# Kernel tuning notes

Hardware: AMD Instinct MI355X
Metric: run time of the kernel (lower is better)

Reference implementation:

```python
import jax, jax.numpy as jnp
import numpy as np


def _sq_cdist(x, y):
    # x: [B,N,D], y: [B,M,D] -> squared L2 distances [B,N,M]
    x_norm = jnp.sum(x * x, axis=-1, keepdims=True)          # [B,N,1]
    y_norm = jnp.sum(y * y, axis=-1, keepdims=True)          # [B,M,1]
    xy = jnp.einsum('bnd,bmd->bnm', x, y)                    # [B,N,M]
    return x_norm - 2.0 * xy + jnp.swapaxes(y_norm, -2, -1)  # [B,N,M]


def setup_inputs() -> dict:
    key = jax.random.key(0)
    kx, ky = jax.random.split(key)
    B, N, M, D = 8, 8192, 8192, 3
    x = jax.random.normal(kx, (B, N, D), dtype=jnp.float32)
    y = jax.random.normal(ky, (B, M, D), dtype=jnp.float32)
    return {"x": x, "y": y}


def reference(x, y):
    d = _sq_cdist(x, y)  # [B,N,M] squared distances (no sqrt, matching original)
    # original d was [B,M,N]; min(dim=2)->per-y-point min over N, min(dim=1)->per-x-point min over M
    per_y = jnp.min(d, axis=1)  # [B,M]
    per_x = jnp.min(d, axis=2)  # [B,N]
    return jnp.mean(per_y) + jnp.mean(per_x)
```

## Files before the change

kernel.cpp:

```cpp
#include <hip/hip_runtime.h>
#include <math.h>


#define B_      8
#define N_      8192
#define Q_      4
#define S_      16
#define CHUNK_  (N_ / S_)


__global__ __launch_bounds__(256)
void minpass_kernel(const float* __restrict__ x, const float* __restrict__ y,
                    float* __restrict__ partX, float* __restrict__ partY) {
    __shared__ float4 sq[CHUNK_];

    const int b    = blockIdx.y;
    const int z    = blockIdx.z;
    const int pass = z >> 4;
    const int s    = z & (S_ - 1);

    const float* qpts = pass ? y : x;
    const float* tpts = pass ? x : y;
    float*       part = pass ? partY : partX;

    {
        const float* tb = tpts + ((long)b * N_ + s * CHUNK_) * 3;
        const float* p  = tb + 6 * threadIdx.x;
        float a0 = p[0], a1 = p[1], a2 = p[2];
        float a3 = p[3], a4 = p[4], a5 = p[5];
        sq[2 * threadIdx.x + 0] = make_float4(-2.0f * a0, -2.0f * a1, -2.0f * a2,
                                              fmaf(a0, a0, fmaf(a1, a1, a2 * a2)));
        sq[2 * threadIdx.x + 1] = make_float4(-2.0f * a3, -2.0f * a4, -2.0f * a5,
                                              fmaf(a3, a3, fmaf(a4, a4, a5 * a5)));
    }
    __syncthreads();

    const int iq0 = (blockIdx.x * blockDim.x + threadIdx.x) * Q_;
    const float4* qp4 = (const float4*)(qpts + ((long)b * N_ + iq0) * 3);
    const float4 f0 = qp4[0];
    const float4 f1 = qp4[1];
    const float4 f2 = qp4[2];
    const float qx[Q_] = {f0.x, f0.w, f1.z, f2.y};
    const float qy[Q_] = {f0.y, f1.x, f1.w, f2.z};
    const float qz[Q_] = {f0.z, f1.y, f2.x, f2.w};

    float m[Q_];
#pragma unroll
    for (int i = 0; i < Q_; ++i) m[i] = __builtin_inff();

    for (int j = 0; j < CHUNK_; j += 4) {
        const float4 ta = sq[j + 0];
        const float4 tb = sq[j + 1];
        const float4 tc = sq[j + 2];
        const float4 td = sq[j + 3];
#pragma unroll
        for (int i = 0; i < Q_; ++i) {
            float sa = fmaf(qx[i], ta.x, fmaf(qy[i], ta.y, fmaf(qz[i], ta.z, ta.w)));
            float sb = fmaf(qx[i], tb.x, fmaf(qy[i], tb.y, fmaf(qz[i], tb.z, tb.w)));
            float sc = fmaf(qx[i], tc.x, fmaf(qy[i], tc.y, fmaf(qz[i], tc.z, tc.w)));
            float sd = fmaf(qx[i], td.x, fmaf(qy[i], td.y, fmaf(qz[i], td.z, td.w)));
            float t  = fminf(fminf(sa, sb), sc);
            m[i]     = fminf(fminf(t, sd), m[i]);
        }
    }

    float4 d;
    {
        float xn0 = fmaf(qx[0], qx[0], fmaf(qy[0], qy[0], qz[0] * qz[0]));
        float xn1 = fmaf(qx[1], qx[1], fmaf(qy[1], qy[1], qz[1] * qz[1]));
        float xn2 = fmaf(qx[2], qx[2], fmaf(qy[2], qy[2], qz[2] * qz[2]));
        float xn3 = fmaf(qx[3], qx[3], fmaf(qy[3], qy[3], qz[3] * qz[3]));
        d.x = fmaxf(m[0] + xn0, 0.0f);
        d.y = fmaxf(m[1] + xn1, 0.0f);
        d.z = fmaxf(m[2] + xn2, 0.0f);
        d.w = fmaxf(m[3] + xn3, 0.0f);
    }
    *(float4*)(part + (long)s * (B_ * N_) + (long)b * N_ + iq0) = d;
}

__global__ __launch_bounds__(256)
void merge_kernel(const float* __restrict__ partX, const float* __restrict__ partY,
                  float* __restrict__ bsum, int BN) {
    const int g = blockIdx.x * blockDim.x + threadIdx.x;
    const float* base = (g < BN) ? (partX + g) : (partY + (g - BN));

    float m = __builtin_inff();
#pragma unroll
    for (int s = 0; s < S_; ++s)
        m = fminf(m, base[(long)s * BN]);

    for (int off = 32; off > 0; off >>= 1)
        m += __shfl_down(m, off, 64);
    __shared__ float wsum[4];
    const int lane = threadIdx.x & 63;
    const int w    = threadIdx.x >> 6;
    if (lane == 0) wsum[w] = m;
    __syncthreads();
    if (threadIdx.x == 0)
        bsum[blockIdx.x] = (wsum[0] + wsum[1]) + (wsum[2] + wsum[3]);
}

__global__ __launch_bounds__(64)
void final_kernel(const float* __restrict__ bsum, float* __restrict__ out,
                  int nb, float scale) {
    float s = 0.0f;
    for (int k = threadIdx.x; k < nb; k += 64)
        s += bsum[k];
    for (int off = 32; off > 0; off >>= 1)
        s += __shfl_down(s, off, 64);
    if (threadIdx.x == 0) out[0] = s * scale;
}

extern "C" void kernel_launch(void* const* d_in, const int* in_sizes, int n_in,
                              void* d_out, int out_size, void* d_ws, size_t ws_size,
                              hipStream_t stream) {
    const float* x = (const float*)d_in[0];
    const float* y = (const float*)d_in[1];
    float* out = (float*)d_out;

    const int BN = B_ * N_;

    float* partX = (float*)d_ws;
    float* partY = partX + (size_t)S_ * BN;
    float* bsum  = partY + (size_t)S_ * BN;

    minpass_kernel<<<dim3(N_ / (256 * Q_), B_, 2 * S_), 256, 0, stream>>>(x, y, partX, partY);

    const int nb = 2 * BN / 256;
    merge_kernel<<<nb, 256, 0, stream>>>(partX, partY, bsum, BN);
    final_kernel<<<1, 64, 0, stream>>>(bsum, out, nb, 1.0f / 65536.0f);
}
```

Measured before the change: 139.9 us.

## Compute pairwise distance terms with split-bf16 MFMA instead of scalar FMAs

Moves the inner distance computation onto matrix cores. Each coordinate is split into bf16 hi/lo parts so the dot product and norm term are computed near fp32 precision with two 16x16x32 bf16 MFMAs per 16x16 tile. A prep kernel packs the target points into MFMA fragment layout in global memory, and the split count drops from 16 to 2, shrinking the merge pass. This risks small precision loss and wasted MFMA lanes, since most of the K dimension is zero padding, and it adds an extra kernel launch.

Measured after the change: 155.7 us. +11.3%, slower.

```diff
diff --git a/kernel.cpp b/kernel.cpp
--- a/kernel.cpp
+++ b/kernel.cpp
@@ -1,100 +1,154 @@
 #include <hip/hip_runtime.h>
 #include <math.h>
+#include <stdint.h>
 
 
-#define B_      8
-#define N_      8192
-#define Q_      4
-#define S_      16
-#define CHUNK_  (N_ / S_)
+#define B_  8
+#define N_  8192
 
+typedef short  s16x8 __attribute__((ext_vector_type(8)));
+typedef float  f32x4 __attribute__((ext_vector_type(4)));
+typedef int    i32x4 __attribute__((ext_vector_type(4)));
+
+__device__ __forceinline__ unsigned bf16rn(float f) {
+    unsigned u = __float_as_uint(f);
+    return (u + 0x7FFFu + ((u >> 16) & 1u)) >> 16;
+}
+__device__ __forceinline__ float bf16tof(unsigned h) {
+    return __uint_as_float(h << 16);
+}
+__device__ __forceinline__ int pk2(unsigned lo, unsigned hi) {
+    return (int)(lo | (hi << 16));
+}
+union frag_u { i32x4 i; s16x8 h; };
+__device__ __forceinline__ s16x8 mkfrag(int w0, int w1, int w2, int w3) {
+    frag_u u; u.i = (i32x4){w0, w1, w2, w3}; return u.h;
+}
+
+__global__ void prep_kernel(const float* __restrict__ x, const float* __restrict__ y,
+                            char* __restrict__ AX, char* __restrict__ AY) {
+    int i = blockIdx.x * blockDim.x + threadIdx.x;
+    if (i >= 2 * B_ * N_) return;
+    const float* src = (i < B_ * N_) ? x : y;
+    char* A = (i < B_ * N_) ? AX : AY;
+    int idx = i & (B_ * N_ - 1);
+    const float* p = src + (long)idx * 3;
+    float t0 = p[0], t1 = p[1], t2 = p[2];
+    float a0 = -2.f * t0, a1 = -2.f * t1, a2 = -2.f * t2;
+    unsigned h0 = bf16rn(a0), h1 = bf16rn(a1), h2 = bf16rn(a2);
+    unsigned l0 = bf16rn(a0 - bf16tof(h0));
+    unsigned l1 = bf16rn(a1 - bf16tof(h1));
+    unsigned l2 = bf16rn(a2 - bf16tof(h2));
+    float tn = fmaf(t0, t0, fmaf(t1, t1, t2 * t2));
+    unsigned nh = bf16rn(tn);
+    unsigned nl = bf16rn(tn - bf16tof(nh));
+    int tile = idx >> 4, r = idx & 15;
+    char* base = A + ((long)tile << 9) + (r << 3);
+    *(int2*)(base      ) = make_int2(pk2(h0, h1), pk2(h2, h0));
+    *(int2*)(base + 128) = make_int2(pk2(h1, h2), pk2(l0, l1));
+    *(int2*)(base + 256) = make_int2(pk2(l2, l0), pk2(l1, l2));
+    *(int2*)(base + 384) = make_int2(pk2(nh, nl), 0);
+}
 
 __global__ __launch_bounds__(256)
 void minpass_kernel(const float* __restrict__ x, const float* __restrict__ y,
+                    const char* __restrict__ AX, const char* __restrict__ AY,
                     float* __restrict__ partX, float* __restrict__ partY) {
-    __shared__ float4 sq[CHUNK_];
+    __shared__ float minbuf[4][128];
+    const int qb   = blockIdx.x;
+    const int b    = blockIdx.y;
+    const int sblk = blockIdx.z & 1;
+    const int dir  = blockIdx.z >> 1;
+    const float* qpts = dir ? y : x;
+    const char*  Ab   = dir ? AX : AY;
+    float*       part = dir ? partY : partX;
 
-    const int b    = blockIdx.y;
-    const int z    = blockIdx.z;
-    const int pass = z >> 4;
-    const int s    = z & (S_ - 1);
+    const int tid = threadIdx.x;
+    const int l   = tid & 63;
+    const int wv  = tid >> 6;
+    const int g   = l >> 4;
+    const int c   = l & 15;
+    const int s   = sblk * 4 + wv;
 
-    const float* qpts = pass ? y : x;
-    const float* tpts = pass ? x : y;
-    float*       part = pass ? partY : partX;
+    s16x8 b1[8], b2[8];
+    const int ONE2 = pk2(0x3F80u, 0x3F80u);
+    #pragma unroll
+    for (int f = 0; f < 8; ++f) {
+        const float* qp = qpts + (long)(b * N_ + qb * 128 + f * 16 + c) * 3;
+        float q0 = qp[0], q1 = qp[1], q2 = qp[2];
+        unsigned h0 = bf16rn(q0), h1 = bf16rn(q1), h2 = bf16rn(q2);
+        unsigned u0 = bf16rn(q0 - bf16tof(h0));
+        unsigned u1 = bf16rn(q1 - bf16tof(h1));
+        unsigned u2 = bf16rn(q2 - bf16tof(h2));
+        int w0 = pk2(h0, h1), w1 = pk2(h2, u0);
+        int w2 = pk2(u1, u2), w3 = pk2(h0, h1);
+        b1[f] = mkfrag(g == 0 ? w0 : 0, g == 0 ? w1 : 0,
+                       g == 3 ? w2 : 0, g == 3 ? w3 : 0);
+        int v0 = pk2(h2, u0), v1 = pk2(u1, u2);
+        b2[f] = mkfrag(g == 0 ? v0 : 0, g == 0 ? v1 : 0,
+                       g == 3 ? ONE2 : 0, 0);
+    }
 
-    {
-        const float* tb = tpts + ((long)b * N_ + s * CHUNK_) * 3;
-        const float* p  = tb + 6 * threadIdx.x;
-        float a0 = p[0], a1 = p[1], a2 = p[2];
-        float a3 = p[3], a4 = p[4], a5 = p[5];
-        sq[2 * threadIdx.x + 0] = make_float4(-2.0f * a0, -2.0f * a1, -2.0f * a2,
-                                              fmaf(a0, a0, fmaf(a1, a1, a2 * a2)));
-        sq[2 * threadIdx.x + 1] = make_float4(-2.0f * a3, -2.0f * a4, -2.0f * a5,
-                                              fmaf(a3, a3, fmaf(a4, a4, a5 * a5)));
+    float m[8];
+    #pragma unroll
+    for (int f = 0; f < 8; ++f) m[f] = __builtin_inff();
+
+    const bool gsel = (g == 0) || (g == 3);
+    const int  goff = (g == 3) ? 128 : 0;
+    const char* pa = Ab + ((long)(b * 512 + s * 64) << 9) + goff + (c << 3);
+
+    int2 c1 = make_int2(0, 0), c2 = make_int2(0, 0);
+    if (gsel) { c1 = *(const int2*)(pa); c2 = *(const int2*)(pa + 256); }
+
+    for (int t = 0; t < 64; ++t) {
+        int2 n1 = make_int2(0, 0), n2 = make_int2(0, 0);
+        const char* pn = pa + ((long)(t + 1) << 9);
+        if (gsel) { n1 = *(const int2*)(pn); n2 = *(const int2*)(pn + 256); }
+
+        s16x8 a1 = mkfrag(g == 0 ? c1.x : 0, g == 0 ? c1.y : 0,
+                          g == 3 ? c1.x : 0, g == 3 ? c1.y : 0);
+        s16x8 a2 = mkfrag(g == 0 ? c2.x : 0, g == 0 ? c2.y : 0,
+                          g == 3 ? c2.x : 0, g == 3 ? c2.y : 0);
+        #pragma unroll
+        for (int f = 0; f < 8; ++f) {
+            f32x4 acc = __builtin_amdgcn_mfma_f32_16x16x32_bf16(
+                a1, b1[f], (f32x4){0.f, 0.f, 0.f, 0.f}, 0, 0, 0);
+            acc = __builtin_amdgcn_mfma_f32_16x16x32_bf16(a2, b2[f], acc, 0, 0, 0);
+            float u = fminf(fminf(acc.x, acc.y), acc.z);
+            m[f] = fminf(fminf(u, acc.w), m[f]);
+        }
+        c1 = n1; c2 = n2;
+    }
+
+    #pragma unroll
+    for (int f = 0; f < 8; ++f) {
+        m[f] = fminf(m[f], __shfl_xor(m[f], 16, 64));
+        m[f] = fminf(m[f], __shfl_xor(m[f], 32, 64));
+    }
+    if (l < 16) {
+        #pragma unroll
+        for (int f = 0; f < 8; ++f) minbuf[wv][f * 16 + l] = m[f];
     }
     __syncthreads();
-
-    const int iq0 = (blockIdx.x * blockDim.x + threadIdx.x) * Q_;
-    const float4* qp4 = (const float4*)(qpts + ((long)b * N_ + iq0) * 3);
-    const float4 f0 = qp4[0];
-    const float4 f1 = qp4[1];
-    const float4 f2 = qp4[2];
-    const float qx[Q_] = {f0.x, f0.w, f1.z, f2.y};
-    const float qy[Q_] = {f0.y, f1.x, f1.w, f2.z};
-    const float qz[Q_] = {f0.z, f1.y, f2.x, f2.w};
-
-    float m[Q_];
-#pragma unroll
-    for (int i = 0; i < Q_; ++i) m[i] = __builtin_inff();
-
-    for (int j = 0; j < CHUNK_; j += 4) {
-        const float4 ta = sq[j + 0];
-        const float4 tb = sq[j + 1];
-        const float4 tc = sq[j + 2];
-        const float4 td = sq[j + 3];
-#pragma unroll
-        for (int i = 0; i < Q_; ++i) {
-            float sa = fmaf(qx[i], ta.x, fmaf(qy[i], ta.y, fmaf(qz[i], ta.z, ta.w)));
-            float sb = fmaf(qx[i], tb.x, fmaf(qy[i], tb.y, fmaf(qz[i], tb.z, tb.w)));
-            float sc = fmaf(qx[i], tc.x, fmaf(qy[i], tc.y, fmaf(qz[i], tc.z, tc.w)));
-            float sd = fmaf(qx[i], td.x, fmaf(qy[i], td.y, fmaf(qz[i], td.z, td.w)));
-            float t  = fminf(fminf(sa, sb), sc);
-            m[i]     = fminf(fminf(t, sd), m[i]);
-        }
+    if (tid < 128) {
+        float v = fminf(fminf(minbuf[0][tid], minbuf[1][tid]),
+                        fminf(minbuf[2][tid], minbuf[3][tid]));
+        const float* qp = qpts + (long)(b * N_ + qb * 128 + tid) * 3;
+        float xn = fmaf(qp[0], qp[0], fmaf(qp[1], qp[1], qp[2] * qp[2]));
+        part[sblk * (B_ * N_) + b * N_ + qb * 128 + tid] = fmaxf(v + xn, 0.f);
     }
-
-    float4 d;
-    {
-        float xn0 = fmaf(qx[0], qx[0], fmaf(qy[0], qy[0], qz[0] * qz[0]));
-        float xn1 = fmaf(qx[1], qx[1], fmaf(qy[1], qy[1], qz[1] * qz[1]));
-        float xn2 = fmaf(qx[2], qx[2], fmaf(qy[2], qy[2], qz[2] * qz[2]));
-        float xn3 = fmaf(qx[3], qx[3], fmaf(qy[3], qy[3], qz[3] * qz[3]));
-        d.x = fmaxf(m[0] + xn0, 0.0f);
-        d.y = fmaxf(m[1] + xn1, 0.0f);
-        d.z = fmaxf(m[2] + xn2, 0.0f);
-        d.w = fmaxf(m[3] + xn3, 0.0f);
-    }
-    *(float4*)(part + (long)s * (B_ * N_) + (long)b * N_ + iq0) = d;
 }
 
 __global__ __launch_bounds__(256)
 void merge_kernel(const float* __restrict__ partX, const float* __restrict__ partY,
                   float* __restrict__ bsum, int BN) {
-    const int g = blockIdx.x * blockDim.x + threadIdx.x;
-    const float* base = (g < BN) ? (partX + g) : (partY + (g - BN));
-
-    float m = __builtin_inff();
-#pragma unroll
-    for (int s = 0; s < S_; ++s)
-        m = fminf(m, base[(long)s * BN]);
-
+    const int gq = blockIdx.x * blockDim.x + threadIdx.x;
+    const float* base = (gq < BN) ? (partX + gq) : (partY + (gq - BN));
+    float mv = fminf(base[0], base[BN]);
     for (int off = 32; off > 0; off >>= 1)
-        m += __shfl_down(m, off, 64);
+        mv += __shfl_down(mv, off, 64);
     __shared__ float wsum[4];
-    const int lane = threadIdx.x & 63;
-    const int w    = threadIdx.x >> 6;
-    if (lane == 0) wsum[w] = m;
+    if ((threadIdx.x & 63) == 0) wsum[threadIdx.x >> 6] = mv;
     __syncthreads();
     if (threadIdx.x == 0)
         bsum[blockIdx.x] = (wsum[0] + wsum[1]) + (wsum[2] + wsum[3]);
@@ -118,14 +172,18 @@
     const float* y = (const float*)d_in[1];
     float* out = (float*)d_out;
 
+    const size_t ASZ = (size_t)(B_ * N_ / 16) * 512 + 512;
+    char*  AX    = (char*)d_ws;
+    char*  AY    = AX + ASZ;
+    float* partX = (float*)(AY + ASZ);
+    float* partY = partX + 2 * (B_ * N_);
+    float* bsum  = partY + 2 * (B_ * N_);
+
+    prep_kernel<<<(2 * B_ * N_ + 255) / 256, 256, 0, stream>>>(x, y, AX, AY);
+
+    minpass_kernel<<<dim3(64, B_, 4), 256, 0, stream>>>(x, y, AX, AY, partX, partY);
+
     const int BN = B_ * N_;
-
-    float* partX = (float*)d_ws;
-    float* partY = partX + (size_t)S_ * BN;
-    float* bsum  = partY + (size_t)S_ * BN;
-
-    minpass_kernel<<<dim3(N_ / (256 * Q_), B_, 2 * S_), 256, 0, stream>>>(x, y, partX, partY);
-
     const int nb = 2 * BN / 256;
     merge_kernel<<<nb, 256, 0, stream>>>(partX, partY, bsum, BN);
     final_kernel<<<1, 64, 0, stream>>>(bsum, out, nb, 1.0f / 65536.0f);
```
